# Performance work log

Measured on AMD Instinct MI355X. Metric: run time of the kernel, lower is better.

## Reference

```python
import jax, jax.numpy as jnp
import numpy as np

B, N = 256, 65536          # batch, num_tokens (world.num_tokens == N)
VOCAB = 50257
ALPHA = 0.5                # dirichlet concentration
EPS = 1e-7                 # gumbel eps


def setup_inputs() -> dict:
    key = jax.random.key(0)
    kb, kt, ku, kd = jax.random.split(key, 4)
    batch = jax.random.randint(kb, (B, N), 0, VOCAB, dtype=jnp.int32)
    t = jax.random.uniform(kt, (B,), dtype=jnp.float32)
    U = jax.random.uniform(ku, (B, N), dtype=jnp.float32)
    # dirichlet(alpha=0.5) sample over the token axis, one simplex per row
    D = jax.random.dirichlet(kd, ALPHA * jnp.ones((N,), jnp.float32), shape=(B,)).astype(jnp.float32)
    return {"batch": batch, "t": t, "U": U, "D": D}


def cosine_schedule(t):
    return 1.0 - jnp.cos(jnp.pi * t / 2)


def cosine_weight(t, eps=1e-3):
    t_adj = t * (1 - 2 * eps) + eps
    return 0.5 * jnp.pi * jnp.sin(jnp.pi * t_adj / 2)


def binary_topk(weights, ks):
    # weights: [B, N] float; ks: [B, 1] int -> bool mask marking the top-k per row
    Bn, Nn = weights.shape
    idx = jnp.argsort(-weights, axis=-1)                     # descending order indices
    rank = jnp.broadcast_to(jnp.arange(Nn), (Bn, Nn))        # rank of each sorted slot
    mask = jnp.zeros((Bn, Nn), dtype=bool)
    mask = mask.at[jnp.arange(Bn)[:, None], idx].set(ks > rank)
    return mask


def reference(batch, t, U, D):
    r = cosine_schedule(t)                                   # mask rate per sample [B]
    w = cosine_weight(t)                                     # loss weight per sample [B]
    G = -jnp.log(-jnp.log(U + EPS) + EPS)                    # gumbel noise [B, N]
    weights = G + jnp.log(D)                                 # gumbel + log-dirichlet
    ks = (N * r).astype(jnp.int32)[:, None]                  # [B, 1] tokens to mask
    mask = binary_topk(weights, ks)                          # [B, N] bool
    return mask, w
```

## Files before the change

kernel.cpp:

```cpp
#include <hip/hip_runtime.h>
#include <math.h>

#define BB 256
#define NN 65536
#define NT 1024
#define SM 4096
#define RANKPAD 160
#define CAPC 8192
#define CAPB 2048
#define QMARG 2e-3f

typedef float f32x4 __attribute__((ext_vector_type(4)));
typedef unsigned int u32x4 __attribute__((ext_vector_type(4)));

#define ONE_BITS 0x3F800000u

__device__ __forceinline__ unsigned int f2sort(float f) {
    unsigned int b = __float_as_uint(f);
    return (b & 0x80000000u) ? ~b : (b | 0x80000000u);
}
__device__ __forceinline__ float sort2f(unsigned int u) {
    unsigned int b = (u & 0x80000000u) ? (u & 0x7fffffffu) : ~u;
    return __uint_as_float(b);
}

__device__ __forceinline__ unsigned int wexact(float u, float d) {
    float t1 = u + 1e-7f;
    float t2 = (float)log((double)t1);
    float t3 = (-t2) + 1e-7f;
    float G  = -(float)log((double)t3);
    float lgD = (float)log((double)d);
    return f2sort(G + lgD);
}

__device__ __forceinline__ unsigned int qkey(float u, float d) {
    float t3 = 1e-7f - __logf(u + 1e-7f);
    float q  = d * __builtin_amdgcn_rcpf(t3);
    return f2sort(q);
}

__device__ __forceinline__ bool finite_f(float f) {
    return (__float_as_uint(f) & 0x7f800000u) != 0x7f800000u;
}

#define PASS1SEL(KKV) \
    { const int b0 = tid * 8; unsigned int cs = 0; \
      _Pragma("unroll") for (int i = 0; i < 8; i++) cs += hist[b0 + i]; \
      chunkSum[tid] = cs; } \
    __syncthreads(); \
    if (tid < 64) { \
        const int c0i = lane * 16; unsigned int s = 0; \
        _Pragma("unroll") for (int i = 0; i < 16; i++) s += chunkSum[c0i + i]; \
        unsigned int suf = s; \
        _Pragma("unroll") for (int off = 1; off < 64; off <<= 1) { \
            unsigned int tv = __shfl_down(suf, off); if (lane + off < 64) suf += tv; } \
        unsigned int above = suf - s; \
        if (suf >= (KKV) && above < (KKV)) { \
            unsigned int cum = above; \
            for (int ci = c0i + 15; ci >= c0i; ci--) { \
                unsigned int cch = chunkSum[ci]; \
                if (cum + cch >= (KKV)) { \
                    for (int b = ci * 8 + 7; ; b--) { \
                        unsigned int c2 = hist[b]; \
                        if (cum + c2 >= (KKV)) { s_sel = (unsigned int)b; s_kneed = (KKV) - cum; s_eq = c2; break; } \
                        cum += c2; } \
                    break; } \
                cum += cch; } } } \
    __syncthreads();

#define PASS2SEL(P, KN) \
    if (tid < 64) { \
        const int c0i = lane * 16; unsigned int s = 0; \
        _Pragma("unroll") for (int i = 0; i < 16; i++) s += hist[c0i + i]; \
        unsigned int suf = s; \
        _Pragma("unroll") for (int off = 1; off < 64; off <<= 1) { \
            unsigned int tv = __shfl_down(suf, off); if (lane + off < 64) suf += tv; } \
        unsigned int above = suf - s; \
        if (suf >= (KN) && above < (KN)) { \
            unsigned int cum = above; \
            for (int b = c0i + 15; ; b--) { \
                unsigned int c2 = hist[b]; \
                if (cum + c2 >= (KN)) { s_sel = ((P) << 10) | (unsigned int)b; s_kneed = (KN) - cum; s_eq = c2; break; } \
                cum += c2; } } } \
    __syncthreads();

#define PASS3SEL(P, KN) \
    if (tid < 64) { \
        const int c0i = lane * 8; unsigned int s = 0; \
        _Pragma("unroll") for (int i = 0; i < 8; i++) s += hist[c0i + i]; \
        unsigned int suf = s; \
        _Pragma("unroll") for (int off = 1; off < 64; off <<= 1) { \
            unsigned int tv = __shfl_down(suf, off); if (lane + off < 64) suf += tv; } \
        unsigned int above = suf - s; \
        if (suf >= (KN) && above < (KN)) { \
            unsigned int cum = above; \
            for (int b = c0i + 7; ; b--) { \
                unsigned int c2 = hist[b]; \
                if (cum + c2 >= (KN)) { s_sel = ((P) << 9) | (unsigned int)b; s_kneed = (KN) - cum; s_eq = c2; break; } \
                cum += c2; } } } \
    __syncthreads();

__global__ __launch_bounds__(NT, 4)
void md_fused_kernel(const float* __restrict__ Tt,
                     const float* __restrict__ U,
                     const float* __restrict__ D,
                     float* __restrict__ out,
                     float* __restrict__ wout) {
    const int row = blockIdx.x;
    const int tid = threadIdx.x;
    const int lane = tid & 63;

    const float* Ur = U + (size_t)row * NN;
    const float* Dr = D + (size_t)row * NN;
    unsigned int* OrU = (unsigned int*)out + (size_t)row * NN;

    __shared__ unsigned int hist[8192];
    __shared__ unsigned int chunkSum[NT];
    __shared__ unsigned int skey[SM];
    __shared__ unsigned int candKey[CAPC];
    __shared__ int candIdx[CAPC];
    __shared__ unsigned int s_sel, s_kneed, s_eq;
    __shared__ int s_A, s_candCnt, s_bandCnt, s_above, s_tiecnt, s_tieidx;

    unsigned int* bandU = skey;
    int* bandIdxA = (int*)(skey + CAPB);
    int* tielist = candIdx;

    const float t = Tt[row];
    const float pf = (float)M_PI;
    float aa = pf * t;
    float bbv = aa * 0.5f;
    float c0 = (float)cos((double)bbv);
    float r  = 1.0f - c0;
    const int k = (int)(65536.0f * r);
    if (tid == 0) {
        float tadj = t * 0.998f + 0.001f;
        float arg  = (pf * tadj) * 0.5f;
        wout[row] = (float)(0.5 * M_PI) * (float)sin((double)arg);
    }

    if (k <= 0 || k >= NN) {
        const unsigned int fbv = (k >= NN) ? ONE_BITS : 0u;
        u32x4 f4 = {fbv, fbv, fbv, fbv};
        for (int j = 0; j < 16; j++)
            __builtin_nontemporal_store(f4, (u32x4*)(OrU + j * 4096 + tid * 4));
        return;
    }
    const unsigned int kk = (unsigned int)k;

    for (int i = tid; i < 8192; i += NT) hist[i] = 0;
    if (tid == 0) { s_A = 0; s_candCnt = 0; s_bandCnt = 0; s_above = 0; }
    __syncthreads();
    {
        float4 u4 = *(const float4*)(Ur + (tid << 2));
        float4 d4 = *(const float4*)(Dr + (tid << 2));
        unsigned int s0 = qkey(u4.x, d4.x), s1 = qkey(u4.y, d4.y);
        unsigned int s2 = qkey(u4.z, d4.z), s3 = qkey(u4.w, d4.w);
        skey[(tid << 2) + 0] = s0; skey[(tid << 2) + 1] = s1;
        skey[(tid << 2) + 2] = s2; skey[(tid << 2) + 3] = s3;
        atomicAdd(&hist[s0 >> 19], 1u); atomicAdd(&hist[s1 >> 19], 1u);
        atomicAdd(&hist[s2 >> 19], 1u); atomicAdd(&hist[s3 >> 19], 1u);
    }
    __syncthreads();

    const int rh = (k >> 4) - RANKPAD;
    unsigned int hi_pivot_u = 0xFFFFFFFFu;
    if (rh >= 1) {
        PASS1SEL((unsigned int)rh)
        const unsigned int bh = s_sel; const unsigned int knh = s_kneed;
        hist[tid] = 0;
        __syncthreads();
        for (int j = tid; j < SM; j += NT) { unsigned int sk = skey[j];
            if ((sk >> 19) == bh) atomicAdd(&hist[(sk >> 9) & 1023u], 1u); }
        __syncthreads();
        PASS2SEL(bh, knh)
        hi_pivot_u = (s_sel << 9) | 0x1FFu;
        for (int i = tid; i < 8192; i += NT) hist[i] = 0;
        __syncthreads();
        for (int j = tid; j < SM; j += NT) atomicAdd(&hist[skey[j] >> 19], 1u);
        __syncthreads();
    }

    const int rl = ((k + 15) >> 4) + RANKPAD;
    unsigned int lo_pivot_u = 0u;
    if (rl <= SM) {
        PASS1SEL((unsigned int)rl)
        const unsigned int bl = s_sel; const unsigned int knl = s_kneed;
        hist[tid] = 0;
        __syncthreads();
        for (int j = tid; j < SM; j += NT) { unsigned int sk = skey[j];
            if ((sk >> 19) == bl) atomicAdd(&hist[(sk >> 9) & 1023u], 1u); }
        __syncthreads();
        PASS2SEL(bl, knl)
        lo_pivot_u = (s_sel << 9);
    }
    __syncthreads();

    {
        int cntA = 0;
#pragma unroll 2
        for (int J = 0; J < 16; ++J) {
            const int e = (J << 12) + (tid << 2);
            float4 u4 = *(const float4*)(Ur + e);
            float4 d4 = *(const float4*)(Dr + e);
            u32x4 kv;
            kv.x = qkey(u4.x, d4.x); kv.y = qkey(u4.y, d4.y);
            kv.z = qkey(u4.z, d4.z); kv.w = qkey(u4.w, d4.w);
            u32x4 m;
#define MPROC(KC, CI, MF) { \
            const unsigned int qv = (KC); \
            const bool din = qv > hi_pivot_u; \
            cntA += (int)din; MF = din ? ONE_BITS : 0u; \
            const bool isc = (!din) && (qv > lo_pivot_u); \
            const unsigned long long mb = __ballot(isc); \
            if (mb) { \
                const int ldr = __ffsll((unsigned long long)mb) - 1; \
                int wbase = 0; \
                if (lane == ldr) wbase = atomicAdd(&s_candCnt, __popcll(mb)); \
                wbase = __shfl(wbase, ldr); \
                if (isc) { \
                    const int slot = wbase + __popcll(mb & ((1ull << lane) - 1ull)); \
                    if (slot < CAPC) { candKey[slot] = qv; candIdx[slot] = e + (CI); } \
                } } }
            MPROC(kv.x, 0, m.x)
            MPROC(kv.y, 1, m.y)
            MPROC(kv.z, 2, m.z)
            MPROC(kv.w, 3, m.w)
#undef MPROC
            *(u32x4*)(OrU + e) = m;
        }
#pragma unroll
        for (int off = 32; off >= 1; off >>= 1) cntA += __shfl_down(cntA, off);
        if (lane == 0) atomicAdd(&s_A, cntA);
    }
    __syncthreads();

    const int candCnt0 = s_candCnt;
    const int candCnt = candCnt0 > CAPC ? CAPC : candCnt0;
    const int kb = k - s_A;
    bool fb = (candCnt0 > CAPC) || (kb < 1) || (kb > candCnt0);

    unsigned int theta_q = 0, band_lo_u = 0, band_hi_u = 0;
    if (!fb) {
        for (int i = tid; i < 8192; i += NT) hist[i] = 0;
        __syncthreads();
        for (int j = tid; j < candCnt; j += NT) atomicAdd(&hist[candKey[j] >> 19], 1u);
        __syncthreads();
        PASS1SEL((unsigned int)kb)
        const unsigned int c13 = s_sel; const unsigned int ck1 = s_kneed;
        hist[tid] = 0;
        __syncthreads();
        for (int j = tid; j < candCnt; j += NT) { unsigned int ck = candKey[j];
            if ((ck >> 19) == c13) atomicAdd(&hist[(ck >> 9) & 1023u], 1u); }
        __syncthreads();
        PASS2SEL(c13, ck1)
        const unsigned int c23 = s_sel; const unsigned int ck2 = s_kneed;
        if (tid < 512) hist[tid] = 0;
        __syncthreads();
        for (int j = tid; j < candCnt; j += NT) { unsigned int ck = candKey[j];
            if ((ck >> 9) == c23) atomicAdd(&hist[ck & 511u], 1u); }
        __syncthreads();
        PASS3SEL(c23, ck2)
        theta_q = s_sel;

        const float theta_f = sort2f(theta_q);
        band_lo_u = f2sort(theta_f * (1.0f - QMARG));
        band_hi_u = f2sort(theta_f * (1.0f + QMARG));
        { const unsigned int fl = (theta_q >= 0x80000100u) ? (theta_q - 256u) : 0x80000000u;
          if (band_lo_u > fl) band_lo_u = fl;
          const unsigned int fh = theta_q + 256u;
          if (band_hi_u < fh) band_hi_u = fh; }
        fb = !(finite_f(theta_f)) || !(band_hi_u < hi_pivot_u) || !(band_lo_u > lo_pivot_u);
    }

    if (!fb) {
        int ab = 0;
        for (int j = tid; j < candCnt; j += NT) {
            const unsigned int ck = candKey[j];
            if (ck > band_hi_u) ab++;
            else if (ck >= band_lo_u) {
                const int slot = atomicAdd(&s_bandCnt, 1);
                if (slot < CAPB) bandIdxA[slot] = candIdx[j];
            }
        }
#pragma unroll
        for (int off = 32; off >= 1; off >>= 1) ab += __shfl_down(ab, off);
        if (lane == 0) atomicAdd(&s_above, ab);
        __syncthreads();
        const int bandCnt = s_bandCnt;
        const int kb2 = kb - s_above;
        fb = (bandCnt > CAPB) || (kb2 < 0) || (kb2 > bandCnt);

        if (!fb) {
            for (int j = tid; j < bandCnt; j += NT) {
                const int idx = bandIdxA[j];
                bandU[j] = wexact(Ur[idx], Dr[idx]);
            }
            __syncthreads();
            for (int j = tid; j < bandCnt; j += NT) {
                const unsigned int me = bandU[j];
                const int mi = bandIdxA[j];
                int rk = 0;
                for (int i = 0; i < bandCnt; i++) {
                    const unsigned int o = bandU[i];
                    rk += (int)((o > me) || (o == me && bandIdxA[i] < mi));
                }
                if (rk < kb2) OrU[mi] = ONE_BITS;
            }
            for (int j = tid; j < candCnt; j += NT)
                if (candKey[j] > band_hi_u) OrU[candIdx[j]] = ONE_BITS;
            return;
        }
    }

    __syncthreads();
    for (int i = tid; i < 8192; i += NT) hist[i] = 0;
    __syncthreads();
#pragma unroll 1
    for (int J = 0; J < 16; ++J) {
        const int e = (J << 12) + (tid << 2);
        float4 u4 = *(const float4*)(Ur + e);
        float4 d4 = *(const float4*)(Dr + e);
        u32x4 kv;
        kv.x = wexact(u4.x, d4.x);
        kv.y = wexact(u4.y, d4.y);
        kv.z = wexact(u4.z, d4.z);
        kv.w = wexact(u4.w, d4.w);
        *(u32x4*)(OrU + e) = kv;
        atomicAdd(&hist[kv.x >> 19], 1u);
        atomicAdd(&hist[kv.y >> 19], 1u);
        atomicAdd(&hist[kv.z >> 19], 1u);
        atomicAdd(&hist[kv.w >> 19], 1u);
    }
    __syncthreads();

    PASS1SEL(kk)
    const unsigned int q13 = s_sel;
    const unsigned int en1 = s_kneed;
    hist[tid] = 0;
    __syncthreads();
#pragma unroll 1
    for (int J = 0; J < 16; ++J) {
        const int e = (J << 12) + (tid << 2);
        u32x4 kv = *(const u32x4*)(OrU + e);
        if ((kv.x >> 19) == q13) atomicAdd(&hist[(kv.x >> 9) & 1023u], 1u);
        if ((kv.y >> 19) == q13) atomicAdd(&hist[(kv.y >> 9) & 1023u], 1u);
        if ((kv.z >> 19) == q13) atomicAdd(&hist[(kv.z >> 9) & 1023u], 1u);
        if ((kv.w >> 19) == q13) atomicAdd(&hist[(kv.w >> 9) & 1023u], 1u);
    }
    __syncthreads();
    PASS2SEL(q13, en1)

    const unsigned int q23 = s_sel;
    const unsigned int en2 = s_kneed;
    if (tid < 512) hist[tid] = 0;
    __syncthreads();
#pragma unroll 1
    for (int J = 0; J < 16; ++J) {
        const int e = (J << 12) + (tid << 2);
        u32x4 kv = *(const u32x4*)(OrU + e);
        if ((kv.x >> 9) == q23) atomicAdd(&hist[kv.x & 511u], 1u);
        if ((kv.y >> 9) == q23) atomicAdd(&hist[kv.y & 511u], 1u);
        if ((kv.z >> 9) == q23) atomicAdd(&hist[kv.z & 511u], 1u);
        if ((kv.w >> 9) == q23) atomicAdd(&hist[kv.w & 511u], 1u);
    }
    __syncthreads();
    PASS3SEL(q23, en2)

    const unsigned int theta = s_sel;
    const unsigned int kneedF = s_kneed, eqF = s_eq;
    const bool needOrder = (kneedF < eqF);
    int istar = NN;
    if (needOrder) {
        if (tid == 0) s_tiecnt = 0;
        __syncthreads();
#pragma unroll 1
        for (int J = 0; J < 16; ++J) {
            const int e = (J << 12) + (tid << 2);
            u32x4 kv = *(const u32x4*)(OrU + e);
#define TIEV(UU, EIDX) if ((UU) == theta) { \
                int pos = atomicAdd(&s_tiecnt, 1); \
                if (pos < 1024) tielist[pos] = (EIDX); }
            TIEV(kv.x, e + 0)
            TIEV(kv.y, e + 1)
            TIEV(kv.z, e + 2)
            TIEV(kv.w, e + 3)
#undef TIEV
        }
        __syncthreads();
        if (tid == 0) {
            int E = s_tiecnt; if (E > 1024) E = 1024;
            for (int aI = 1; aI < E; aI++) {
                int val = tielist[aI]; int bI = aI - 1;
                while (bI >= 0 && tielist[bI] > val) { tielist[bI + 1] = tielist[bI]; bI--; }
                tielist[bI + 1] = val;
            }
            int kk2 = (int)kneedF; if (kk2 > E) kk2 = E; if (kk2 < 1) kk2 = 1;
            s_tieidx = tielist[kk2 - 1];
        }
        __syncthreads();
        istar = s_tieidx;
    }

#pragma unroll 1
    for (int J = 0; J < 16; ++J) {
        const int e = (J << 12) + (tid << 2);
        u32x4 kv = *(const u32x4*)(OrU + e);
        u32x4 m;
#define MVE(u, idx) ((((u) > theta) || ((u) == theta && (!needOrder || (idx) <= istar))) ? ONE_BITS : 0u)
        m.x = MVE(kv.x, e + 0);
        m.y = MVE(kv.y, e + 1);
        m.z = MVE(kv.z, e + 2);
        m.w = MVE(kv.w, e + 3);
#undef MVE
        *(u32x4*)(OrU + e) = m;
    }
}

extern "C" void kernel_launch(void* const* d_in, const int* in_sizes, int n_in,
                              void* d_out, int out_size, void* d_ws, size_t ws_size,
                              hipStream_t stream) {
    const float* T = (const float*)d_in[1];
    const float* U = (const float*)d_in[2];
    const float* D = (const float*)d_in[3];
    float* out = (float*)d_out;
    float* wout = out + (size_t)BB * NN;

    md_fused_kernel<<<BB, NT, 0, stream>>>(T, U, D, out, wout);
}
```

Before: 230.4 us.

## Split fused per-row kernel into pivot, sliced streaming, and select kernels

Replaces the single one-block-per-row kernel with three kernels. A small pivot kernel computes the hi/lo rank pivots from a 4096-element sample using an 8-bit radix select and writes them to workspace. A streaming kernel with 8 blocks per row writes the definite mask and collects candidates into a global workspace buffer, and a select kernel then resolves the threshold. This spreads the bandwidth-bound main pass over more blocks than the 256 rows give, at the cost of extra launches, global atomics and a workspace round trip. The fused path also swaps wave-aggregated ballot appends for per-element shared atomics, and it remains as a fallback when no workspace is provided.

```diff
diff --git a/kernel.cpp b/kernel.cpp
--- a/kernel.cpp
+++ b/kernel.cpp
@@ -3,10 +3,15 @@
 
 #define BB 256
 #define NN 65536
-#define NT 1024
+#define NTA 256
+#define NTB 256
+#define NTC 1024
+#define SLICES 8
+#define SLICE_ELEMS 8192
 #define SM 4096
 #define RANKPAD 160
 #define CAPC 8192
+#define BCAP 1024
 #define CAPB 2048
 #define QMARG 2e-3f
 
@@ -14,6 +19,15 @@
 typedef unsigned int u32x4 __attribute__((ext_vector_type(4)));
 
 #define ONE_BITS 0x3F800000u
+
+#define WS_K    0
+#define WS_HI   (WS_K + BB)
+#define WS_LO   (WS_HI + BB)
+#define WS_CAND (WS_LO + BB)
+#define WS_A    (WS_CAND + BB)
+#define WS_KEYS (WS_A + BB)
+#define WS_IDX  (WS_KEYS + BB * CAPC)
+#define WS_WORDS ((size_t)WS_IDX + (size_t)BB * CAPC)
 
 __device__ __forceinline__ unsigned int f2sort(float f) {
     unsigned int b = __float_as_uint(f);
@@ -100,7 +114,396 @@
                 cum += c2; } } } \
     __syncthreads();
 
-__global__ __launch_bounds__(NT, 4)
+__device__ __forceinline__ unsigned int rankSelect(const unsigned int* skey,
+        unsigned int* h, unsigned int* s_pfx, int* s_need,
+        const int tid, const int lane, const int r) {
+    if (tid == 0) { *s_pfx = 0u; *s_need = r; }
+    __syncthreads();
+    for (int shift = 24; shift >= 0; shift -= 8) {
+        h[tid] = 0u;
+        __syncthreads();
+        const unsigned int pfx = *s_pfx;
+        const int need = *s_need;
+        for (int j = tid; j < SM; j += NTA) {
+            const unsigned int sk = skey[j];
+            if (shift == 24 || (sk >> (shift + 8)) == (pfx >> (shift + 8)))
+                atomicAdd(&h[(sk >> shift) & 255u], 1u);
+        }
+        __syncthreads();
+        if (tid < 64) {
+            const int b0 = lane * 4;
+            unsigned int s = h[b0] + h[b0 + 1] + h[b0 + 2] + h[b0 + 3];
+            unsigned int suf = s;
+#pragma unroll
+            for (int off = 1; off < 64; off <<= 1) {
+                unsigned int tv = __shfl_down(suf, off);
+                if (lane + off < 64) suf += tv;
+            }
+            const unsigned int above = suf - s;
+            if (suf >= (unsigned int)need && above < (unsigned int)need) {
+                unsigned int cum = above;
+                for (int b = b0 + 3; ; b--) {
+                    const unsigned int c = h[b];
+                    if (cum + c >= (unsigned int)need) {
+                        *s_pfx = pfx | ((unsigned int)b << shift);
+                        *s_need = need - (int)cum;
+                        break;
+                    }
+                    cum += c;
+                }
+            }
+        }
+        __syncthreads();
+    }
+    return *s_pfx;
+}
+
+__global__ __launch_bounds__(NTA)
+void md_pivots(const float* __restrict__ Tt, const float* __restrict__ U,
+               const float* __restrict__ D, unsigned int* __restrict__ ws,
+               float* __restrict__ wout) {
+    const int row = blockIdx.x;
+    const int tid = threadIdx.x;
+    const int lane = tid & 63;
+
+    const float t = Tt[row];
+    const float pf = (float)M_PI;
+    float bbv = (pf * t) * 0.5f;
+    float c0 = (float)cos((double)bbv);
+    const int k = (int)(65536.0f * (1.0f - c0));
+    if (tid == 0) {
+        float tadj = t * 0.998f + 0.001f;
+        float arg = (pf * tadj) * 0.5f;
+        wout[row] = (float)(0.5 * M_PI) * (float)sin((double)arg);
+        ws[WS_K + row] = (unsigned int)k;
+        ((int*)ws)[WS_CAND + row] = 0;
+        ((int*)ws)[WS_A + row] = 0;
+    }
+    if (k <= 0 || k >= NN) {
+        if (tid == 0) { ws[WS_HI + row] = 0xFFFFFFFFu; ws[WS_LO + row] = 0u; }
+        return;
+    }
+
+    __shared__ unsigned int skey[SM];
+    __shared__ unsigned int h[256];
+    __shared__ unsigned int s_pfx;
+    __shared__ int s_need;
+
+    const float* Ur = U + (size_t)row * NN;
+    const float* Dr = D + (size_t)row * NN;
+#pragma unroll
+    for (int g = 0; g < 4; ++g) {
+        const int e = (g << 10) + (tid << 2);
+        float4 u4 = *(const float4*)(Ur + e);
+        float4 d4 = *(const float4*)(Dr + e);
+        skey[e + 0] = qkey(u4.x, d4.x);
+        skey[e + 1] = qkey(u4.y, d4.y);
+        skey[e + 2] = qkey(u4.z, d4.z);
+        skey[e + 3] = qkey(u4.w, d4.w);
+    }
+    __syncthreads();
+
+    const int rh = (k >> 4) - RANKPAD;
+    const int rl = (k >> 4) + RANKPAD;
+    unsigned int hi = 0xFFFFFFFFu;
+    unsigned int lo = 0u;
+    if (rh >= 1)  hi = rankSelect(skey, h, &s_pfx, &s_need, tid, lane, rh);
+    if (rl <= SM) lo = rankSelect(skey, h, &s_pfx, &s_need, tid, lane, rl);
+    if (tid == 0) { ws[WS_HI + row] = hi; ws[WS_LO + row] = lo; }
+}
+
+__global__ __launch_bounds__(NTB)
+void md_stream(const float* __restrict__ U, const float* __restrict__ D,
+               float* __restrict__ out, unsigned int* __restrict__ ws) {
+    const int bid = blockIdx.x;
+    const int row = bid >> 3;
+    const int sl = bid & 7;
+    const int tid = threadIdx.x;
+    const int lane = tid & 63;
+
+    const int k = (int)ws[WS_K + row];
+    unsigned int* OrU = (unsigned int*)out + (size_t)row * NN + (size_t)sl * SLICE_ELEMS;
+    if (k <= 0 || k >= NN) {
+        const unsigned int fv = (k >= NN) ? ONE_BITS : 0u;
+        u32x4 f4 = {fv, fv, fv, fv};
+        for (int J = 0; J < 8; ++J)
+            __builtin_nontemporal_store(f4, (u32x4*)(OrU + (J << 10) + (tid << 2)));
+        return;
+    }
+    const unsigned int hi = ws[WS_HI + row];
+    const unsigned int lo = ws[WS_LO + row];
+    const float* Ur = U + (size_t)row * NN + (size_t)sl * SLICE_ELEMS;
+    const float* Dr = D + (size_t)row * NN + (size_t)sl * SLICE_ELEMS;
+    unsigned int* gk = ws + WS_KEYS + (size_t)row * CAPC;
+    int* gi = (int*)ws + WS_IDX + (size_t)row * CAPC;
+    int* gCand = (int*)ws + WS_CAND + row;
+    int* gA = (int*)ws + WS_A + row;
+
+    __shared__ unsigned int lk[BCAP];
+    __shared__ int li[BCAP];
+    __shared__ int s_cnt, s_base;
+    if (tid == 0) s_cnt = 0;
+    __syncthreads();
+
+    int dcnt = 0;
+    const int ibase = sl * SLICE_ELEMS;
+#pragma unroll 2
+    for (int J = 0; J < 8; ++J) {
+        const int e = (J << 10) + (tid << 2);
+        float4 u4 = *(const float4*)(Ur + e);
+        float4 d4 = *(const float4*)(Dr + e);
+        u32x4 kv;
+        kv.x = qkey(u4.x, d4.x); kv.y = qkey(u4.y, d4.y);
+        kv.z = qkey(u4.z, d4.z); kv.w = qkey(u4.w, d4.w);
+        u32x4 m;
+#define SPROC(QV, CI, MF) { const unsigned int qv = (QV); \
+        const bool din = qv > hi; dcnt += (int)din; MF = din ? ONE_BITS : 0u; \
+        if (!din && qv > lo) { \
+            const int p = atomicAdd(&s_cnt, 1); \
+            if (p < BCAP) { lk[p] = qv; li[p] = ibase + e + (CI); } \
+            else { const int g = atomicAdd(gCand, 1); \
+                   if (g < CAPC) { gk[g] = qv; gi[g] = ibase + e + (CI); } } } }
+        SPROC(kv.x, 0, m.x)
+        SPROC(kv.y, 1, m.y)
+        SPROC(kv.z, 2, m.z)
+        SPROC(kv.w, 3, m.w)
+#undef SPROC
+        *(u32x4*)(OrU + e) = m;
+    }
+#pragma unroll
+    for (int off = 32; off >= 1; off >>= 1) dcnt += __shfl_down(dcnt, off);
+    if (lane == 0 && dcnt) atomicAdd(gA, dcnt);
+    __syncthreads();
+    if (tid == 0) {
+        int n = s_cnt; if (n > BCAP) n = BCAP;
+        s_base = atomicAdd(gCand, n);
+    }
+    __syncthreads();
+    {
+        int n = s_cnt; if (n > BCAP) n = BCAP;
+        for (int j = tid; j < n; j += NTB) {
+            const int g = s_base + j;
+            if (g < CAPC) { gk[g] = lk[j]; gi[g] = li[j]; }
+        }
+    }
+}
+
+__global__ __launch_bounds__(NTC)
+void md_select(const float* __restrict__ U, const float* __restrict__ D,
+               float* __restrict__ out, unsigned int* __restrict__ ws) {
+    const int row = blockIdx.x;
+    const int tid = threadIdx.x;
+    const int lane = tid & 63;
+
+    const int k = (int)ws[WS_K + row];
+    if (k <= 0 || k >= NN) return;
+    const unsigned int kk = (unsigned int)k;
+
+    const float* Ur = U + (size_t)row * NN;
+    const float* Dr = D + (size_t)row * NN;
+    unsigned int* OrU = (unsigned int*)out + (size_t)row * NN;
+
+    const unsigned int hi_u = ws[WS_HI + row];
+    const unsigned int lo_u = ws[WS_LO + row];
+    const int candCnt0 = ((int*)ws)[WS_CAND + row];
+    const int A = ((int*)ws)[WS_A + row];
+    const unsigned int* gk = ws + WS_KEYS + (size_t)row * CAPC;
+    const int* gi = (const int*)ws + WS_IDX + (size_t)row * CAPC;
+
+    __shared__ unsigned int hist[8192];
+    __shared__ unsigned int chunkSum[NTC];
+    __shared__ unsigned int candKey[CAPC];
+    __shared__ int candIdx[CAPC];
+    __shared__ unsigned int bandU[CAPB];
+    __shared__ int bandIdxA[CAPB];
+    __shared__ unsigned int s_sel, s_kneed, s_eq;
+    __shared__ int s_bandCnt, s_above, s_tiecnt, s_tieidx;
+    int* tielist = candIdx;
+
+    const int kb = k - A;
+    bool fb = (candCnt0 > CAPC) || (kb < 1) || (kb > candCnt0);
+    const int candCnt = candCnt0 > CAPC ? CAPC : candCnt0;
+
+    unsigned int theta_q = 0, band_lo_u = 0, band_hi_u = 0;
+    if (!fb) {
+        if (tid == 0) { s_bandCnt = 0; s_above = 0; }
+        for (int j = tid; j < candCnt; j += NTC) { candKey[j] = gk[j]; candIdx[j] = gi[j]; }
+        for (int i = tid; i < 8192; i += NTC) hist[i] = 0;
+        __syncthreads();
+        for (int j = tid; j < candCnt; j += NTC) atomicAdd(&hist[candKey[j] >> 19], 1u);
+        __syncthreads();
+        PASS1SEL((unsigned int)kb)
+        const unsigned int c13 = s_sel; const unsigned int ck1 = s_kneed;
+        hist[tid] = 0;
+        __syncthreads();
+        for (int j = tid; j < candCnt; j += NTC) { unsigned int ck = candKey[j];
+            if ((ck >> 19) == c13) atomicAdd(&hist[(ck >> 9) & 1023u], 1u); }
+        __syncthreads();
+        PASS2SEL(c13, ck1)
+        const unsigned int c23 = s_sel; const unsigned int ck2 = s_kneed;
+        if (tid < 512) hist[tid] = 0;
+        __syncthreads();
+        for (int j = tid; j < candCnt; j += NTC) { unsigned int ck = candKey[j];
+            if ((ck >> 9) == c23) atomicAdd(&hist[ck & 511u], 1u); }
+        __syncthreads();
+        PASS3SEL(c23, ck2)
+        theta_q = s_sel;
+
+        const float theta_f = sort2f(theta_q);
+        band_lo_u = f2sort(theta_f * (1.0f - QMARG));
+        band_hi_u = f2sort(theta_f * (1.0f + QMARG));
+        { const unsigned int fl = (theta_q >= 0x80000100u) ? (theta_q - 256u) : 0x80000000u;
+          if (band_lo_u > fl) band_lo_u = fl;
+          const unsigned int fh = theta_q + 256u;
+          if (band_hi_u < fh) band_hi_u = fh; }
+        fb = !(finite_f(theta_f)) || !(band_hi_u < hi_u) || !(band_lo_u > lo_u);
+    }
+
+    if (!fb) {
+        int ab = 0;
+        for (int j = tid; j < candCnt; j += NTC) {
+            const unsigned int ck = candKey[j];
+            if (ck > band_hi_u) ab++;
+            else if (ck >= band_lo_u) {
+                const int slot = atomicAdd(&s_bandCnt, 1);
+                if (slot < CAPB) bandIdxA[slot] = candIdx[j];
+            }
+        }
+#pragma unroll
+        for (int off = 32; off >= 1; off >>= 1) ab += __shfl_down(ab, off);
+        if (lane == 0) atomicAdd(&s_above, ab);
+        __syncthreads();
+        const int bandCnt = s_bandCnt;
+        const int kb2 = kb - s_above;
+        fb = (bandCnt > CAPB) || (kb2 < 0) || (kb2 > bandCnt);
+
+        if (!fb) {
+            for (int j = tid; j < bandCnt; j += NTC) {
+                const int idx = bandIdxA[j];
+                bandU[j] = wexact(Ur[idx], Dr[idx]);
+            }
+            __syncthreads();
+            for (int j = tid; j < bandCnt; j += NTC) {
+                const unsigned int me = bandU[j];
+                const int mi = bandIdxA[j];
+                int rk = 0;
+                for (int i = 0; i < bandCnt; i++) {
+                    const unsigned int o = bandU[i];
+                    rk += (int)((o > me) || (o == me && bandIdxA[i] < mi));
+                }
+                if (rk < kb2) OrU[mi] = ONE_BITS;
+            }
+            for (int j = tid; j < candCnt; j += NTC)
+                if (candKey[j] > band_hi_u) OrU[candIdx[j]] = ONE_BITS;
+            return;
+        }
+    }
+
+    __syncthreads();
+    for (int i = tid; i < 8192; i += NTC) hist[i] = 0;
+    __syncthreads();
+#pragma unroll 1
+    for (int J = 0; J < 16; ++J) {
+        const int e = (J << 12) + (tid << 2);
+        float4 u4 = *(const float4*)(Ur + e);
+        float4 d4 = *(const float4*)(Dr + e);
+        u32x4 kv;
+        kv.x = wexact(u4.x, d4.x);
+        kv.y = wexact(u4.y, d4.y);
+        kv.z = wexact(u4.z, d4.z);
+        kv.w = wexact(u4.w, d4.w);
+        *(u32x4*)(OrU + e) = kv;
+        atomicAdd(&hist[kv.x >> 19], 1u);
+        atomicAdd(&hist[kv.y >> 19], 1u);
+        atomicAdd(&hist[kv.z >> 19], 1u);
+        atomicAdd(&hist[kv.w >> 19], 1u);
+    }
+    __syncthreads();
+
+    PASS1SEL(kk)
+    const unsigned int q13 = s_sel;
+    const unsigned int en1 = s_kneed;
+    hist[tid] = 0;
+    __syncthreads();
+#pragma unroll 1
+    for (int J = 0; J < 16; ++J) {
+        const int e = (J << 12) + (tid << 2);
+        u32x4 kv = *(const u32x4*)(OrU + e);
+        if ((kv.x >> 19) == q13) atomicAdd(&hist[(kv.x >> 9) & 1023u], 1u);
+        if ((kv.y >> 19) == q13) atomicAdd(&hist[(kv.y >> 9) & 1023u], 1u);
+        if ((kv.z >> 19) == q13) atomicAdd(&hist[(kv.z >> 9) & 1023u], 1u);
+        if ((kv.w >> 19) == q13) atomicAdd(&hist[(kv.w >> 9) & 1023u], 1u);
+    }
+    __syncthreads();
+    PASS2SEL(q13, en1)
+
+    const unsigned int q23 = s_sel;
+    const unsigned int en2 = s_kneed;
+    if (tid < 512) hist[tid] = 0;
+    __syncthreads();
+#pragma unroll 1
+    for (int J = 0; J < 16; ++J) {
+        const int e = (J << 12) + (tid << 2);
+        u32x4 kv = *(const u32x4*)(OrU + e);
+        if ((kv.x >> 9) == q23) atomicAdd(&hist[kv.x & 511u], 1u);
+        if ((kv.y >> 9) == q23) atomicAdd(&hist[kv.y & 511u], 1u);
+        if ((kv.z >> 9) == q23) atomicAdd(&hist[kv.z & 511u], 1u);
+        if ((kv.w >> 9) == q23) atomicAdd(&hist[kv.w & 511u], 1u);
+    }
+    __syncthreads();
+    PASS3SEL(q23, en2)
+
+    const unsigned int theta = s_sel;
+    const unsigned int kneedF = s_kneed, eqF = s_eq;
+    const bool needOrder = (kneedF < eqF);
+    int istar = NN;
+    if (needOrder) {
+        if (tid == 0) s_tiecnt = 0;
+        __syncthreads();
+#pragma unroll 1
+        for (int J = 0; J < 16; ++J) {
+            const int e = (J << 12) + (tid << 2);
+            u32x4 kv = *(const u32x4*)(OrU + e);
+#define TIEV(UU, EIDX) if ((UU) == theta) { \
+                int pos = atomicAdd(&s_tiecnt, 1); \
+                if (pos < 1024) tielist[pos] = (EIDX); }
+            TIEV(kv.x, e + 0)
+            TIEV(kv.y, e + 1)
+            TIEV(kv.z, e + 2)
+            TIEV(kv.w, e + 3)
+#undef TIEV
+        }
+        __syncthreads();
+        if (tid == 0) {
+            int E = s_tiecnt; if (E > 1024) E = 1024;
+            for (int aI = 1; aI < E; aI++) {
+                int val = tielist[aI]; int bI = aI - 1;
+                while (bI >= 0 && tielist[bI] > val) { tielist[bI + 1] = tielist[bI]; bI--; }
+                tielist[bI + 1] = val;
+            }
+            int kk2 = (int)kneedF; if (kk2 > E) kk2 = E; if (kk2 < 1) kk2 = 1;
+            s_tieidx = tielist[kk2 - 1];
+        }
+        __syncthreads();
+        istar = s_tieidx;
+    }
+
+#pragma unroll 1
+    for (int J = 0; J < 16; ++J) {
+        const int e = (J << 12) + (tid << 2);
+        u32x4 kv = *(const u32x4*)(OrU + e);
+        u32x4 m;
+#define MVE(u, idx) ((((u) > theta) || ((u) == theta && (!needOrder || (idx) <= istar))) ? ONE_BITS : 0u)
+        m.x = MVE(kv.x, e + 0);
+        m.y = MVE(kv.y, e + 1);
+        m.z = MVE(kv.z, e + 2);
+        m.w = MVE(kv.w, e + 3);
+#undef MVE
+        *(u32x4*)(OrU + e) = m;
+    }
+}
+
+__global__ __launch_bounds__(NTC, 4)
 void md_fused_kernel(const float* __restrict__ Tt,
                      const float* __restrict__ U,
                      const float* __restrict__ D,
@@ -115,7 +518,7 @@
     unsigned int* OrU = (unsigned int*)out + (size_t)row * NN;
 
     __shared__ unsigned int hist[8192];
-    __shared__ unsigned int chunkSum[NT];
+    __shared__ unsigned int chunkSum[NTC];
     __shared__ unsigned int skey[SM];
     __shared__ unsigned int candKey[CAPC];
     __shared__ int candIdx[CAPC];
@@ -128,11 +531,9 @@
 
     const float t = Tt[row];
     const float pf = (float)M_PI;
-    float aa = pf * t;
-    float bbv = aa * 0.5f;
+    float bbv = (pf * t) * 0.5f;
     float c0 = (float)cos((double)bbv);
-    float r  = 1.0f - c0;
-    const int k = (int)(65536.0f * r);
+    const int k = (int)(65536.0f * (1.0f - c0));
     if (tid == 0) {
         float tadj = t * 0.998f + 0.001f;
         float arg  = (pf * tadj) * 0.5f;
@@ -148,7 +549,7 @@
     }
     const unsigned int kk = (unsigned int)k;
 
-    for (int i = tid; i < 8192; i += NT) hist[i] = 0;
+    for (int i = tid; i < 8192; i += NTC) hist[i] = 0;
     if (tid == 0) { s_A = 0; s_candCnt = 0; s_bandCnt = 0; s_above = 0; }
     __syncthreads();
     {
@@ -170,14 +571,14 @@
         const unsigned int bh = s_sel; const unsigned int knh = s_kneed;
         hist[tid] = 0;
         __syncthreads();
-        for (int j = tid; j < SM; j += NT) { unsigned int sk = skey[j];
+        for (int j = tid; j < SM; j += NTC) { unsigned int sk = skey[j];
             if ((sk >> 19) == bh) atomicAdd(&hist[(sk >> 9) & 1023u], 1u); }
         __syncthreads();
         PASS2SEL(bh, knh)
         hi_pivot_u = (s_sel << 9) | 0x1FFu;
-        for (int i = tid; i < 8192; i += NT) hist[i] = 0;
-        __syncthreads();
-        for (int j = tid; j < SM; j += NT) atomicAdd(&hist[skey[j] >> 19], 1u);
+        for (int i = tid; i < 8192; i += NTC) hist[i] = 0;
+        __syncthreads();
+        for (int j = tid; j < SM; j += NTC) atomicAdd(&hist[skey[j] >> 19], 1u);
         __syncthreads();
     }
 
@@ -188,7 +589,7 @@
         const unsigned int bl = s_sel; const unsigned int knl = s_kneed;
         hist[tid] = 0;
         __syncthreads();
-        for (int j = tid; j < SM; j += NT) { unsigned int sk = skey[j];
+        for (int j = tid; j < SM; j += NTC) { unsigned int sk = skey[j];
             if ((sk >> 19) == bl) atomicAdd(&hist[(sk >> 9) & 1023u], 1u); }
         __syncthreads();
         PASS2SEL(bl, knl)
@@ -211,17 +612,9 @@
             const unsigned int qv = (KC); \
             const bool din = qv > hi_pivot_u; \
             cntA += (int)din; MF = din ? ONE_BITS : 0u; \
-            const bool isc = (!din) && (qv > lo_pivot_u); \
-            const unsigned long long mb = __ballot(isc); \
-            if (mb) { \
-                const int ldr = __ffsll((unsigned long long)mb) - 1; \
-                int wbase = 0; \
-                if (lane == ldr) wbase = atomicAdd(&s_candCnt, __popcll(mb)); \
-                wbase = __shfl(wbase, ldr); \
-                if (isc) { \
-                    const int slot = wbase + __popcll(mb & ((1ull << lane) - 1ull)); \
-                    if (slot < CAPC) { candKey[slot] = qv; candIdx[slot] = e + (CI); } \
-                } } }
+            if (!din && qv > lo_pivot_u) { \
+                int slot = atomicAdd(&s_candCnt, 1); \
+                if (slot < CAPC) { candKey[slot] = qv; candIdx[slot] = e + (CI); } } }
             MPROC(kv.x, 0, m.x)
             MPROC(kv.y, 1, m.y)
             MPROC(kv.z, 2, m.z)
@@ -242,22 +635,22 @@
 
     unsigned int theta_q = 0, band_lo_u = 0, band_hi_u = 0;
     if (!fb) {
-        for (int i = tid; i < 8192; i += NT) hist[i] = 0;
-        __syncthreads();
-        for (int j = tid; j < candCnt; j += NT) atomicAdd(&hist[candKey[j] >> 19], 1u);
+        for (int i = tid; i < 8192; i += NTC) hist[i] = 0;
+        __syncthreads();
+        for (int j = tid; j < candCnt; j += NTC) atomicAdd(&hist[candKey[j] >> 19], 1u);
         __syncthreads();
         PASS1SEL((unsigned int)kb)
         const unsigned int c13 = s_sel; const unsigned int ck1 = s_kneed;
         hist[tid] = 0;
         __syncthreads();
-        for (int j = tid; j < candCnt; j += NT) { unsigned int ck = candKey[j];
+        for (int j = tid; j < candCnt; j += NTC) { unsigned int ck = candKey[j];
             if ((ck >> 19) == c13) atomicAdd(&hist[(ck >> 9) & 1023u], 1u); }
         __syncthreads();
         PASS2SEL(c13, ck1)
         const unsigned int c23 = s_sel; const unsigned int ck2 = s_kneed;
         if (tid < 512) hist[tid] = 0;
         __syncthreads();
-        for (int j = tid; j < candCnt; j += NT) { unsigned int ck = candKey[j];
+        for (int j = tid; j < candCnt; j += NTC) { unsigned int ck = candKey[j];
             if ((ck >> 9) == c23) atomicAdd(&hist[ck & 511u], 1u); }
         __syncthreads();
         PASS3SEL(c23, ck2)
@@ -275,7 +668,7 @@
 
     if (!fb) {
         int ab = 0;
-        for (int j = tid; j < candCnt; j += NT) {
+        for (int j = tid; j < candCnt; j += NTC) {
             const unsigned int ck = candKey[j];
             if (ck > band_hi_u) ab++;
             else if (ck >= band_lo_u) {
@@ -292,12 +685,12 @@
         fb = (bandCnt > CAPB) || (kb2 < 0) || (kb2 > bandCnt);
 
         if (!fb) {
-            for (int j = tid; j < bandCnt; j += NT) {
+            for (int j = tid; j < bandCnt; j += NTC) {
                 const int idx = bandIdxA[j];
                 bandU[j] = wexact(Ur[idx], Dr[idx]);
             }
             __syncthreads();
-            for (int j = tid; j < bandCnt; j += NT) {
+            for (int j = tid; j < bandCnt; j += NTC) {
                 const unsigned int me = bandU[j];
                 const int mi = bandIdxA[j];
                 int rk = 0;
@@ -307,14 +700,14 @@
                 }
                 if (rk < kb2) OrU[mi] = ONE_BITS;
             }
-            for (int j = tid; j < candCnt; j += NT)
+            for (int j = tid; j < candCnt; j += NTC)
                 if (candKey[j] > band_hi_u) OrU[candIdx[j]] = ONE_BITS;
             return;
         }
     }
 
     __syncthreads();
-    for (int i = tid; i < 8192; i += NT) hist[i] = 0;
+    for (int i = tid; i < 8192; i += NTC) hist[i] = 0;
     __syncthreads();
 #pragma unroll 1
     for (int J = 0; J < 16; ++J) {
@@ -426,5 +819,12 @@
     float* out = (float*)d_out;
     float* wout = out + (size_t)BB * NN;
 
-    md_fused_kernel<<<BB, NT, 0, stream>>>(T, U, D, out, wout);
-}
+    if (d_ws != nullptr && ws_size >= WS_WORDS * 4ull) {
+        unsigned int* ws = (unsigned int*)d_ws;
+        md_pivots<<<BB, NTA, 0, stream>>>(T, U, D, ws, wout);
+        md_stream<<<BB * SLICES, NTB, 0, stream>>>(U, D, out, ws);
+        md_select<<<BB, NTC, 0, stream>>>(U, D, out, ws);
+    } else {
+        md_fused_kernel<<<BB, NTC, 0, stream>>>(T, U, D, out, wout);
+    }
+}
```

Result: slower. 248.4 us (+7.8%).
